# Optimization experiments

Measured on AMD Instinct MI355X. Metric: run time of the kernel, lower is better.

## Reference

```python
import jax, jax.numpy as jnp
import numpy as np

RMS_EPS = 1e-6


def setup_inputs() -> dict:
    key = jax.random.key(0)
    ks = jax.random.split(key, 6)
    B, S, D, F, E = 4, 2048, 1024, 4096, 8
    scale = 0.02
    return {
        "hidden_states": jax.random.normal(ks[0], (B, S, D), dtype=jnp.float32),
        "norm_weight": jnp.ones((D,), dtype=jnp.float32),
        "gate_w": jax.random.normal(ks[1], (E, D), dtype=jnp.float32) * scale,
        "w1": jax.random.normal(ks[2], (E, D, F), dtype=jnp.float32) * scale,
        "w3": jax.random.normal(ks[3], (E, D, F), dtype=jnp.float32) * scale,
        "w2": jax.random.normal(ks[4], (E, F, D), dtype=jnp.float32) * scale,
        "top_k": 2,
    }


def reference(hidden_states, norm_weight, gate_w, w1, w3, w2, top_k):
    B, S, D = hidden_states.shape
    E = gate_w.shape[0]
    # norm_fn: RMSNorm (pre-MoE norm in Mixtral block)
    x = hidden_states * jax.lax.rsqrt(jnp.mean(jnp.square(hidden_states), axis=-1, keepdims=True) + RMS_EPS)
    x = (x * norm_weight).reshape(-1, D)  # [T, D], T = B*S
    # router
    router_logits = jnp.einsum('td,ed->te', x, gate_w)  # [T, E]
    routing = jax.nn.softmax(router_logits.astype(jnp.float32), axis=-1)
    top_w, top_idx = jax.lax.top_k(routing, top_k)  # [T, k]
    top_w = top_w / jnp.sum(top_w, axis=-1, keepdims=True)
    top_w = top_w.astype(x.dtype)
    # dense-masked expert combine: tokens not routed to expert e get weight 0,
    # mathematically identical to the gather/scatter loop in the original.
    out = jnp.zeros_like(x)
    for e in range(E):  # fixed small loop over experts
        w_e = jnp.sum(jnp.where(top_idx == e, top_w, 0.0), axis=-1)  # [T]
        h = jax.nn.silu(x @ w1[e]) * (x @ w3[e])  # [T, F] SwiGLU expert
        out = out + w_e[:, None] * (h @ w2[e])
    return out.reshape(B, S, D), router_logits
```

## Files before the change

### kernel.cpp

```cpp
#include <hip/hip_runtime.h>
#include <hip/hip_bf16.h>

#define T_TOK 8192
#define D_DIM 1024
#define F_DIM 4096
#define E_NUM 8

typedef short s16x8 __attribute__((ext_vector_type(8)));
typedef float f32x4 __attribute__((ext_vector_type(4)));
typedef unsigned short u16x8 __attribute__((ext_vector_type(8)));

__device__ __forceinline__ unsigned short f2bf(float f) {
  union { float f; unsigned int u; } v; v.f = f;
  unsigned int u = v.u;
  return (unsigned short)((u + 0x7FFFu + ((u >> 16) & 1u)) >> 16);
}

__device__ __forceinline__ void async16(const void* g, void* l) {
  __builtin_amdgcn_global_load_lds((const __attribute__((address_space(1))) void*)g,
                                   (__attribute__((address_space(3))) void*)l, 16, 0, 0);
}

__global__ __launch_bounds__(256) void prepass_kernel(
    const float* __restrict__ hs, const float* __restrict__ nw,
    const float* __restrict__ gw, const float* __restrict__ w1,
    const float* __restrict__ w3, const float* __restrict__ w2,
    unsigned short* __restrict__ xb, unsigned short* __restrict__ w13t,
    unsigned short* __restrict__ w2t, float* __restrict__ logits_out,
    int* __restrict__ cnt, int* __restrict__ ilist, float* __restrict__ wlist) {
  __shared__ unsigned short tileS[64][72];
  __shared__ float red[4];
  __shared__ float pl[4][8];
  int bx = blockIdx.x;
  int tid = threadIdx.x;
  if (bx < 24576) {
    int tensor = bx >> 13;
    int e = (bx >> 10) & 7;
    int tl = bx & 1023;
    const float* src; int C, tr, tc;
    if (tensor == 0) {
      src = w1 + (size_t)e * D_DIM * F_DIM; C = F_DIM; tr = tl >> 6; tc = tl & 63;
    } else if (tensor == 1) {
      src = w3 + (size_t)e * D_DIM * F_DIM; C = F_DIM; tr = tl >> 6; tc = tl & 63;
    } else {
      src = w2 + (size_t)e * F_DIM * D_DIM; C = D_DIM; tr = tl >> 4; tc = tl & 15;
    }
    int r0 = tr * 64, c0 = tc * 64;
    int rr = tid >> 4, ccb = (tid & 15) * 4;
#pragma unroll
    for (int i = 0; i < 4; ++i) {
      int r = rr + i * 16;
      float4 v = *(const float4*)(src + (size_t)(r0 + r) * C + c0 + ccb);
      tileS[ccb + 0][r] = f2bf(v.x);
      tileS[ccb + 1][r] = f2bf(v.y);
      tileS[ccb + 2][r] = f2bf(v.z);
      tileS[ccb + 3][r] = f2bf(v.w);
    }
    __syncthreads();
    int row = tid >> 2, col = (tid & 3) * 16;
    unsigned short* dp;
    if (tensor < 2) {
      int f = c0 + row;
      int prow = ((f >> 5) * 64) + (f & 31) + (tensor == 1 ? 32 : 0);
      dp = w13t + ((size_t)e * 8192 + prow) * D_DIM + r0 + col;
    } else {
      dp = w2t + ((size_t)e * D_DIM + c0 + row) * F_DIM + r0 + col;
    }
    u16x8 v0, v1;
#pragma unroll
    for (int j = 0; j < 8; ++j) { v0[j] = tileS[row][col + j]; v1[j] = tileS[row][col + 8 + j]; }
    *(u16x8*)dp = v0;
    *(u16x8*)(dp + 8) = v1;
  } else {
    int t = bx - 24576;
    int lane = tid & 63, wid = tid >> 6;
    float4 v = ((const float4*)(hs + (size_t)t * D_DIM))[tid];
    float ss = v.x * v.x + v.y * v.y + v.z * v.z + v.w * v.w;
#pragma unroll
    for (int o = 32; o > 0; o >>= 1) ss += __shfl_xor(ss, o);
    if (lane == 0) red[wid] = ss;
    __syncthreads();
    float ms = (red[0] + red[1] + red[2] + red[3]) * (1.0f / 1024.0f);
    float rs = rsqrtf(ms + 1e-6f);
    float4 wv = ((const float4*)nw)[tid];
    float x0 = v.x * rs * wv.x, x1 = v.y * rs * wv.y;
    float x2 = v.z * rs * wv.z, x3 = v.w * rs * wv.w;
    ((ushort4*)(xb + (size_t)t * D_DIM))[tid] =
        make_ushort4(f2bf(x0), f2bf(x1), f2bf(x2), f2bf(x3));
    float p[8];
#pragma unroll
    for (int e = 0; e < 8; ++e) {
      float4 g = ((const float4*)(gw + (size_t)e * D_DIM))[tid];
      p[e] = x0 * g.x + x1 * g.y + x2 * g.z + x3 * g.w;
    }
#pragma unroll
    for (int e = 0; e < 8; ++e) {
#pragma unroll
      for (int o = 32; o > 0; o >>= 1) p[e] += __shfl_xor(p[e], o);
    }
    if (lane == 0) {
#pragma unroll
      for (int e = 0; e < 8; ++e) pl[wid][e] = p[e];
    }
    __syncthreads();
    if (tid == 0) {
      float l[8];
#pragma unroll
      for (int e = 0; e < 8; ++e) {
        l[e] = pl[0][e] + pl[1][e] + pl[2][e] + pl[3][e];
        logits_out[(size_t)t * 8 + e] = l[e];
      }
      int i0 = 0; float b0 = l[0];
#pragma unroll
      for (int e = 1; e < 8; ++e) if (l[e] > b0) { b0 = l[e]; i0 = e; }
      int i1 = (i0 == 0) ? 1 : 0; float b1 = l[i1];
#pragma unroll
      for (int e = 0; e < 8; ++e) if (e != i0 && l[e] > b1) { b1 = l[e]; i1 = e; }
      float wa = 1.0f / (1.0f + __expf(b1 - b0));
      float wb = 1.0f / (1.0f + __expf(b0 - b1));
      int p0 = atomicAdd(&cnt[i0], 1);
      ilist[i0 * T_TOK + p0] = t * 2;     wlist[i0 * T_TOK + p0] = wa;
      int p1 = atomicAdd(&cnt[i1], 1);
      ilist[i1 * T_TOK + p1] = t * 2 + 1; wlist[i1 * T_TOK + p1] = wb;
    }
  }
}

__global__ __launch_bounds__(512, 2) void gemm1_kernel(
    const unsigned short* __restrict__ xb, const unsigned short* __restrict__ w13t,
    unsigned short* __restrict__ H, const int* __restrict__ cnt,
    const int* __restrict__ ilist) {
  int flat = blockIdx.x;
  int e = flat & 7;
  int widx = flat >> 3;
  int ne = cnt[e];
  int art = (ne + 255) >> 8;
  if (widx >= (art << 5)) return;
  int rt = widx % art;
  int ft = widx / art;
  int r0 = rt * 256;
  __shared__ __align__(16) unsigned short As[3 * 8192];
  __shared__ __align__(16) unsigned short Bs[3 * 8192];
  __shared__ int toks[256];
  int tid = threadIdx.x, lane = tid & 63, w = tid >> 6;
  if (tid < 256) toks[tid] = ilist[e * T_TOK + min(r0 + tid, ne - 1)];
  __syncthreads();
  const unsigned short* bpanel = w13t + ((size_t)e * 8192 + ft * 256) * D_DIM;
  int sr0 = tid >> 2, sr1 = sr0 + 128;
  int ch0 = (((tid & 3) ^ ((sr0 >> 1) & 3)) * 8);
  int ch1 = (((tid & 3) ^ ((sr1 >> 1) & 3)) * 8);
  const unsigned short* ap0 = xb + (size_t)(toks[sr0] >> 1) * D_DIM + ch0;
  const unsigned short* ap1 = xb + (size_t)(toks[sr1] >> 1) * D_DIM + ch1;
  const unsigned short* bp0 = bpanel + (size_t)sr0 * D_DIM + ch0;
  const unsigned short* bp1 = bpanel + (size_t)sr1 * D_DIM + ch1;
  int d0 = (sr0 * 32) + (tid & 3) * 8;
  int d1 = d0 + 4096;
  int wr = w >> 2, wc = w & 3;
  int lr = lane & 15, lc = lane >> 4;
  int aoff[8], boff[4];
#pragma unroll
  for (int m = 0; m < 8; ++m) {
    int row = wr * 128 + m * 16 + lr;
    aoff[m] = row * 32 + ((lc ^ ((row >> 1) & 3)) * 8);
  }
#pragma unroll
  for (int n = 0; n < 4; ++n) {
    int row = wc * 64 + n * 16 + lr;
    boff[n] = row * 32 + ((lc ^ ((row >> 1) & 3)) * 8);
  }
  f32x4 acc[8][4] = {};
  async16(ap0, &As[d0]); async16(ap1, &As[d1]);
  async16(bp0, &Bs[d0]); async16(bp1, &Bs[d1]);
  async16(ap0 + 32, &As[8192 + d0]); async16(ap1 + 32, &As[8192 + d1]);
  async16(bp0 + 32, &Bs[8192 + d0]); async16(bp1 + 32, &Bs[8192 + d1]);

#define G1_STEP(T_, BUF_, VMC_, DOST_)                                          \
  {                                                                             \
    asm volatile("s_waitcnt vmcnt(" VMC_ ")" ::: "memory");                     \
    __builtin_amdgcn_s_barrier();                                               \
    const unsigned short* Ab = &As[(BUF_) * 8192];                              \
    const unsigned short* Bb = &Bs[(BUF_) * 8192];                              \
    s16x8 a[8], b[4];                                                           \
    if (DOST_) {                                   \
      int nk = ((T_) + 2) * 32;                                                 \
      async16(ap0 + nk, &As[(((BUF_) + 2) % 3) * 8192 + d0]);                   \
      async16(ap1 + nk, &As[(((BUF_) + 2) % 3) * 8192 + d1]);                   \
    }                                                                           \
    _Pragma("unroll") for (int m = 0; m < 4; ++m)                               \
        a[m] = *(const s16x8*)(Ab + aoff[m]);                                   \
    _Pragma("unroll") for (int n = 0; n < 4; ++n)                               \
        b[n] = *(const s16x8*)(Bb + boff[n]);                                   \
    __builtin_amdgcn_s_setprio(1);                                              \
    _Pragma("unroll") for (int m = 0; m < 4; ++m)                               \
        _Pragma("unroll") for (int n = 0; n < 4; ++n)                           \
            acc[m][n] = __builtin_amdgcn_mfma_f32_16x16x32_bf16(                \
                a[m], b[n], acc[m][n], 0, 0, 0);                                \
    __builtin_amdgcn_s_setprio(0);                                              \
    if (DOST_) {                                   \
      int nk = ((T_) + 2) * 32;                                                 \
      async16(bp0 + nk, &Bs[(((BUF_) + 2) % 3) * 8192 + d0]);                   \
      async16(bp1 + nk, &Bs[(((BUF_) + 2) % 3) * 8192 + d1]);                   \
    }                                                                           \
    _Pragma("unroll") for (int m = 4; m < 8; ++m)                               \
        a[m] = *(const s16x8*)(Ab + aoff[m]);                                   \
    __builtin_amdgcn_s_setprio(1);                                              \
    _Pragma("unroll") for (int m = 4; m < 8; ++m)                               \
        _Pragma("unroll") for (int n = 0; n < 4; ++n)                           \
            acc[m][n] = __builtin_amdgcn_mfma_f32_16x16x32_bf16(                \
                a[m], b[n], acc[m][n], 0, 0, 0);                                \
    __builtin_amdgcn_s_setprio(0);                                              \
  }

  for (int tb = 0; tb < 30; tb += 3) {
    G1_STEP(tb, 0, "4", 1)
    G1_STEP(tb + 1, 1, "4", 1)
    G1_STEP(tb + 2, 2, "4", 1)
  }
  G1_STEP(30, 0, "4", 0)
  G1_STEP(31, 1, "0", 0)
#undef G1_STEP

  int g4 = lane >> 4, cl = lane & 15;
  int fbase = (4 * ft + wc) * 32;
#pragma unroll
  for (int m = 0; m < 8; ++m) {
#pragma unroll
    for (int j = 0; j < 4; ++j) {
      int rloc = wr * 128 + m * 16 + g4 * 4 + j;
      if (r0 + rloc < ne) {
        unsigned short* hp = H + (size_t)toks[rloc] * F_DIM + fbase + cl;
#pragma unroll
        for (int n = 0; n < 2; ++n) {
          float c1 = acc[m][n][j], c3 = acc[m][n + 2][j];
          float h = c1 / (1.0f + __expf(-c1)) * c3;
          hp[n * 16] = f2bf(h);
        }
      }
    }
  }
}

__global__ __launch_bounds__(512, 2) void gemm2_kernel(
    const unsigned short* __restrict__ H, const unsigned short* __restrict__ w2t,
    const int* __restrict__ cnt, const int* __restrict__ ilist,
    const float* __restrict__ wlist, float* __restrict__ out) {
  int flat = blockIdx.x;
  int e = flat & 7;
  int widx = flat >> 3;
  int ne = cnt[e];
  int art = (ne + 255) >> 8;
  if (widx >= (art << 2)) return;
  int rt = widx % art;
  int nt = widx / art;
  int r0 = rt * 256;
  __shared__ __align__(16) unsigned short As[3 * 8192];
  __shared__ __align__(16) unsigned short Bs[3 * 8192];
  __shared__ int toks[256];
  __shared__ float wts[256];
  int tid = threadIdx.x, lane = tid & 63, w = tid >> 6;
  if (tid < 256) {
    int idx = e * T_TOK + min(r0 + tid, ne - 1);
    toks[tid] = ilist[idx];
    wts[tid] = wlist[idx];
  }
  __syncthreads();
  const unsigned short* bpanel = w2t + ((size_t)e * D_DIM + nt * 256) * F_DIM;
  int sr0 = tid >> 2, sr1 = sr0 + 128;
  int ch0 = (((tid & 3) ^ ((sr0 >> 1) & 3)) * 8);
  int ch1 = (((tid & 3) ^ ((sr1 >> 1) & 3)) * 8);
  const unsigned short* ap0 = H + (size_t)toks[sr0] * F_DIM + ch0;
  const unsigned short* ap1 = H + (size_t)toks[sr1] * F_DIM + ch1;
  const unsigned short* bp0 = bpanel + (size_t)sr0 * F_DIM + ch0;
  const unsigned short* bp1 = bpanel + (size_t)sr1 * F_DIM + ch1;
  int d0 = (sr0 * 32) + (tid & 3) * 8;
  int d1 = d0 + 4096;
  int wr = w >> 2, wc = w & 3;
  int lr = lane & 15, lc = lane >> 4;
  int aoff[8], boff[4];
#pragma unroll
  for (int m = 0; m < 8; ++m) {
    int row = wr * 128 + m * 16 + lr;
    aoff[m] = row * 32 + ((lc ^ ((row >> 1) & 3)) * 8);
  }
#pragma unroll
  for (int n = 0; n < 4; ++n) {
    int row = wc * 64 + n * 16 + lr;
    boff[n] = row * 32 + ((lc ^ ((row >> 1) & 3)) * 8);
  }
  f32x4 acc[8][4] = {};
  async16(ap0, &As[d0]); async16(ap1, &As[d1]);
  async16(bp0, &Bs[d0]); async16(bp1, &Bs[d1]);
  async16(ap0 + 32, &As[8192 + d0]); async16(ap1 + 32, &As[8192 + d1]);
  async16(bp0 + 32, &Bs[8192 + d0]); async16(bp1 + 32, &Bs[8192 + d1]);

#define G2_STEP(T_, BUF_, VMC_, DOST_)                                          \
  {                                                                             \
    asm volatile("s_waitcnt vmcnt(" VMC_ ")" ::: "memory");                     \
    __builtin_amdgcn_s_barrier();                                               \
    const unsigned short* Ab = &As[(BUF_) * 8192];                              \
    const unsigned short* Bb = &Bs[(BUF_) * 8192];                              \
    s16x8 a[8], b[4];                                                           \
    if (DOST_) {                                                                \
      int nk = ((T_) + 2) * 32;                                                 \
      async16(ap0 + nk, &As[(((BUF_) + 2) % 3) * 8192 + d0]);                   \
      async16(ap1 + nk, &As[(((BUF_) + 2) % 3) * 8192 + d1]);                   \
    }                                                                           \
    _Pragma("unroll") for (int m = 0; m < 4; ++m)                               \
        a[m] = *(const s16x8*)(Ab + aoff[m]);                                   \
    _Pragma("unroll") for (int n = 0; n < 4; ++n)                               \
        b[n] = *(const s16x8*)(Bb + boff[n]);                                   \
    __builtin_amdgcn_s_setprio(1);                                              \
    _Pragma("unroll") for (int m = 0; m < 4; ++m)                               \
        _Pragma("unroll") for (int n = 0; n < 4; ++n)                           \
            acc[m][n] = __builtin_amdgcn_mfma_f32_16x16x32_bf16(                \
                a[m], b[n], acc[m][n], 0, 0, 0);                                \
    __builtin_amdgcn_s_setprio(0);                                              \
    if (DOST_) {                                                                \
      int nk = ((T_) + 2) * 32;                                                 \
      async16(bp0 + nk, &Bs[(((BUF_) + 2) % 3) * 8192 + d0]);                   \
      async16(bp1 + nk, &Bs[(((BUF_) + 2) % 3) * 8192 + d1]);                   \
    }                                                                           \
    _Pragma("unroll") for (int m = 4; m < 8; ++m)                               \
        a[m] = *(const s16x8*)(Ab + aoff[m]);                                   \
    __builtin_amdgcn_s_setprio(1);                                              \
    _Pragma("unroll") for (int m = 4; m < 8; ++m)                               \
        _Pragma("unroll") for (int n = 0; n < 4; ++n)                           \
            acc[m][n] = __builtin_amdgcn_mfma_f32_16x16x32_bf16(                \
                a[m], b[n], acc[m][n], 0, 0, 0);                                \
    __builtin_amdgcn_s_setprio(0);                                              \
  }

  for (int tb = 0; tb < 126; tb += 3) {
    G2_STEP(tb, 0, "4", 1)
    G2_STEP(tb + 1, 1, "4", 1)
    G2_STEP(tb + 2, 2, "4", 1)
  }
  G2_STEP(126, 0, "4", 0)
  G2_STEP(127, 1, "0", 0)
#undef G2_STEP

  int g4 = lane >> 4, cl = lane & 15;
#pragma unroll
  for (int m = 0; m < 8; ++m) {
#pragma unroll
    for (int j = 0; j < 4; ++j) {
      int rloc = wr * 128 + m * 16 + g4 * 4 + j;
      if (r0 + rloc < ne) {
        int tok = toks[rloc] >> 1;
        float ww = wts[rloc];
        float* op = out + (size_t)tok * D_DIM + nt * 256 + wc * 64 + cl;
#pragma unroll
        for (int n = 0; n < 4; ++n)
          unsafeAtomicAdd(op + n * 16, ww * acc[m][n][j]);
      }
    }
  }
}

extern "C" void kernel_launch(void* const* d_in, const int* in_sizes, int n_in,
                              void* d_out, int out_size, void* d_ws, size_t ws_size,
                              hipStream_t stream) {
  const float* hs = (const float*)d_in[0];
  const float* nw = (const float*)d_in[1];
  const float* gw = (const float*)d_in[2];
  const float* w1 = (const float*)d_in[3];
  const float* w3 = (const float*)d_in[4];
  const float* w2 = (const float*)d_in[5];
  float* out = (float*)d_out;
  float* logits_out = out + (size_t)T_TOK * D_DIM;

  char* ws = (char*)d_ws;
  unsigned short* xb   = (unsigned short*)(ws);
  unsigned short* w13t = (unsigned short*)(ws + 16777216ull);
  unsigned short* w2t  = (unsigned short*)(ws + 150994944ull);
  unsigned short* H    = (unsigned short*)(ws + 218103808ull);
  int*   ilist = (int*)(ws + 352321536ull);
  float* wlist = (float*)(ws + 352583680ull);
  int*   cnt   = (int*)(ws + 352845824ull);

  hipMemsetAsync(out, 0, (size_t)T_TOK * D_DIM * sizeof(float), stream);
  hipMemsetAsync(cnt, 0, E_NUM * sizeof(int), stream);
  prepass_kernel<<<24576 + T_TOK, 256, 0, stream>>>(
      hs, nw, gw, w1, w3, w2, xb, w13t, w2t, logits_out, cnt, ilist, wlist);
  gemm1_kernel<<<E_NUM * 32 * 32, 512, 0, stream>>>(xb, w13t, H, cnt, ilist);
  gemm2_kernel<<<E_NUM * 32 * 4, 512, 0, stream>>>(H, w2t, cnt, ilist, wlist, out);
}
```

Baseline: 821.0 us.

## Pre-swizzle expert weights into MFMA fragment order and load B directly to registers

The prepass now writes w13 and w2 in a fragment-major layout, so each lane's 16-byte MFMA B operand sits contiguously per 16-row group and k-step. Both GEMM kernels drop the shared-memory B tiles and issue direct global_load_dwordx4 into registers, keeping only the activation tile in LDS with a triple-buffered async pipeline. This removes the LDS traffic and bank pressure for weights and frees LDS, but exposes global load latency on the MFMA critical path with only a single-step lookahead. Each wave also now loads its own B fragments, with no sharing across waves that use the same columns.

```diff
diff --git a/kernel.cpp b/kernel.cpp
--- a/kernel.cpp
+++ b/kernel.cpp
@@ -62,15 +62,20 @@
     if (tensor < 2) {
       int f = c0 + row;
       int prow = ((f >> 5) * 64) + (f & 31) + (tensor == 1 ? 32 : 0);
-      dp = w13t + ((size_t)e * 8192 + prow) * D_DIM + r0 + col;
+      int d0 = r0 + col;
+      dp = w13t + (size_t)e * 8388608 + (size_t)(prow >> 4) * 16384 +
+           (d0 >> 5) * 512 + ((d0 >> 3) & 3) * 128 + (prow & 15) * 8;
     } else {
-      dp = w2t + ((size_t)e * D_DIM + c0 + row) * F_DIM + r0 + col;
+      int rowD = c0 + row;
+      int k0f = r0 + col;
+      dp = w2t + (size_t)e * 4194304 + (size_t)(rowD >> 4) * 65536 +
+           (k0f >> 5) * 512 + ((k0f >> 3) & 3) * 128 + (rowD & 15) * 8;
     }
     u16x8 v0, v1;
 #pragma unroll
     for (int j = 0; j < 8; ++j) { v0[j] = tileS[row][col + j]; v1[j] = tileS[row][col + 8 + j]; }
     *(u16x8*)dp = v0;
-    *(u16x8*)(dp + 8) = v1;
+    *(u16x8*)(dp + 128) = v1;
   } else {
     int t = bx - 24576;
     int lane = tid & 63, wid = tid >> 6;
@@ -125,6 +130,39 @@
     }
   }
 }
+
+#define BLOAD(B_, P_) \
+  asm volatile("global_load_dwordx4 %0, %1, off" : "=v"(B_) : "v"(P_));
+
+#define GX_STEP(T_, BUF_, VMC_, DOA_)                                           \
+  {                                                                             \
+    const unsigned short* pb0 = bfp0 + (T_) * 512;                              \
+    const unsigned short* pb1 = bfp1 + (T_) * 512;                              \
+    const unsigned short* pb2 = bfp2 + (T_) * 512;                              \
+    const unsigned short* pb3 = bfp3 + (T_) * 512;                              \
+    s16x8 b0, b1, b2, b3;                                                       \
+    BLOAD(b0, pb0) BLOAD(b1, pb1) BLOAD(b2, pb2) BLOAD(b3, pb3)                 \
+    if (DOA_) {                                                                 \
+      int nk = ((T_) + 2) * 32;                                                 \
+      async16(ap0 + nk, &As[(((BUF_) + 2) % 3) * 8192 + d0]);                   \
+      async16(ap1 + nk, &As[(((BUF_) + 2) % 3) * 8192 + d1]);                   \
+    }                                                                           \
+    const unsigned short* Ab = &As[(BUF_) * 8192];                              \
+    s16x8 a[8];                                                                 \
+    _Pragma("unroll") for (int m = 0; m < 8; ++m)                               \
+        a[m] = *(const s16x8*)(Ab + aoff[m]);                                   \
+    asm volatile("s_waitcnt vmcnt(" VMC_ ")" ::: "memory");                     \
+    __builtin_amdgcn_sched_barrier(0);                                          \
+    __builtin_amdgcn_s_setprio(1);                                              \
+    _Pragma("unroll") for (int m = 0; m < 8; ++m) {                             \
+      acc[m][0] = __builtin_amdgcn_mfma_f32_16x16x32_bf16(a[m], b0, acc[m][0], 0, 0, 0); \
+      acc[m][1] = __builtin_amdgcn_mfma_f32_16x16x32_bf16(a[m], b1, acc[m][1], 0, 0, 0); \
+      acc[m][2] = __builtin_amdgcn_mfma_f32_16x16x32_bf16(a[m], b2, acc[m][2], 0, 0, 0); \
+      acc[m][3] = __builtin_amdgcn_mfma_f32_16x16x32_bf16(a[m], b3, acc[m][3], 0, 0, 0); \
+    }                                                                           \
+    __builtin_amdgcn_s_setprio(0);                                              \
+    __builtin_amdgcn_s_barrier();                                               \
+  }
 
 __global__ __launch_bounds__(512, 2) void gemm1_kernel(
     const unsigned short* __restrict__ xb, const unsigned short* __restrict__ w13t,
@@ -140,85 +178,42 @@
   int ft = widx / art;
   int r0 = rt * 256;
   __shared__ __align__(16) unsigned short As[3 * 8192];
-  __shared__ __align__(16) unsigned short Bs[3 * 8192];
   __shared__ int toks[256];
   int tid = threadIdx.x, lane = tid & 63, w = tid >> 6;
   if (tid < 256) toks[tid] = ilist[e * T_TOK + min(r0 + tid, ne - 1)];
   __syncthreads();
-  const unsigned short* bpanel = w13t + ((size_t)e * 8192 + ft * 256) * D_DIM;
   int sr0 = tid >> 2, sr1 = sr0 + 128;
   int ch0 = (((tid & 3) ^ ((sr0 >> 1) & 3)) * 8);
   int ch1 = (((tid & 3) ^ ((sr1 >> 1) & 3)) * 8);
   const unsigned short* ap0 = xb + (size_t)(toks[sr0] >> 1) * D_DIM + ch0;
   const unsigned short* ap1 = xb + (size_t)(toks[sr1] >> 1) * D_DIM + ch1;
-  const unsigned short* bp0 = bpanel + (size_t)sr0 * D_DIM + ch0;
-  const unsigned short* bp1 = bpanel + (size_t)sr1 * D_DIM + ch1;
   int d0 = (sr0 * 32) + (tid & 3) * 8;
   int d1 = d0 + 4096;
   int wr = w >> 2, wc = w & 3;
   int lr = lane & 15, lc = lane >> 4;
-  int aoff[8], boff[4];
+  int aoff[8];
 #pragma unroll
   for (int m = 0; m < 8; ++m) {
     int row = wr * 128 + m * 16 + lr;
     aoff[m] = row * 32 + ((lc ^ ((row >> 1) & 3)) * 8);
   }
-#pragma unroll
-  for (int n = 0; n < 4; ++n) {
-    int row = wc * 64 + n * 16 + lr;
-    boff[n] = row * 32 + ((lc ^ ((row >> 1) & 3)) * 8);
-  }
+  const unsigned short* bbase = w13t + (size_t)e * 8388608 + (size_t)lane * 8;
+  const unsigned short* bfp0 = bbase + (size_t)(ft * 16 + wc * 4 + 0) * 16384;
+  const unsigned short* bfp1 = bbase + (size_t)(ft * 16 + wc * 4 + 1) * 16384;
+  const unsigned short* bfp2 = bbase + (size_t)(ft * 16 + wc * 4 + 2) * 16384;
+  const unsigned short* bfp3 = bbase + (size_t)(ft * 16 + wc * 4 + 3) * 16384;
   f32x4 acc[8][4] = {};
-  async16(ap0, &As[d0]); async16(ap1, &As[d1]);
-  async16(bp0, &Bs[d0]); async16(bp1, &Bs[d1]);
+  async16(ap0, &As[d0]);             async16(ap1, &As[d1]);
   async16(ap0 + 32, &As[8192 + d0]); async16(ap1 + 32, &As[8192 + d1]);
-  async16(bp0 + 32, &Bs[8192 + d0]); async16(bp1 + 32, &Bs[8192 + d1]);
-
-#define G1_STEP(T_, BUF_, VMC_, DOST_)                                          \
-  {                                                                             \
-    asm volatile("s_waitcnt vmcnt(" VMC_ ")" ::: "memory");                     \
-    __builtin_amdgcn_s_barrier();                                               \
-    const unsigned short* Ab = &As[(BUF_) * 8192];                              \
-    const unsigned short* Bb = &Bs[(BUF_) * 8192];                              \
-    s16x8 a[8], b[4];                                                           \
-    if (DOST_) {                                   \
-      int nk = ((T_) + 2) * 32;                                                 \
-      async16(ap0 + nk, &As[(((BUF_) + 2) % 3) * 8192 + d0]);                   \
-      async16(ap1 + nk, &As[(((BUF_) + 2) % 3) * 8192 + d1]);                   \
-    }                                                                           \
-    _Pragma("unroll") for (int m = 0; m < 4; ++m)                               \
-        a[m] = *(const s16x8*)(Ab + aoff[m]);                                   \
-    _Pragma("unroll") for (int n = 0; n < 4; ++n)                               \
-        b[n] = *(const s16x8*)(Bb + boff[n]);                                   \
-    __builtin_amdgcn_s_setprio(1);                                              \
-    _Pragma("unroll") for (int m = 0; m < 4; ++m)                               \
-        _Pragma("unroll") for (int n = 0; n < 4; ++n)                           \
-            acc[m][n] = __builtin_amdgcn_mfma_f32_16x16x32_bf16(                \
-                a[m], b[n], acc[m][n], 0, 0, 0);                                \
-    __builtin_amdgcn_s_setprio(0);                                              \
-    if (DOST_) {                                   \
-      int nk = ((T_) + 2) * 32;                                                 \
-      async16(bp0 + nk, &Bs[(((BUF_) + 2) % 3) * 8192 + d0]);                   \
-      async16(bp1 + nk, &Bs[(((BUF_) + 2) % 3) * 8192 + d1]);                   \
-    }                                                                           \
-    _Pragma("unroll") for (int m = 4; m < 8; ++m)                               \
-        a[m] = *(const s16x8*)(Ab + aoff[m]);                                   \
-    __builtin_amdgcn_s_setprio(1);                                              \
-    _Pragma("unroll") for (int m = 4; m < 8; ++m)                               \
-        _Pragma("unroll") for (int n = 0; n < 4; ++n)                           \
-            acc[m][n] = __builtin_amdgcn_mfma_f32_16x16x32_bf16(                \
-                a[m], b[n], acc[m][n], 0, 0, 0);                                \
-    __builtin_amdgcn_s_setprio(0);                                              \
-  }
-
+  asm volatile("s_waitcnt vmcnt(2)" ::: "memory");
+  __builtin_amdgcn_s_barrier();
   for (int tb = 0; tb < 30; tb += 3) {
-    G1_STEP(tb, 0, "4", 1)
-    G1_STEP(tb + 1, 1, "4", 1)
-    G1_STEP(tb + 2, 2, "4", 1)
-  }
-  G1_STEP(30, 0, "4", 0)
-  G1_STEP(31, 1, "0", 0)
-#undef G1_STEP
+    GX_STEP(tb, 0, "2", 1)
+    GX_STEP(tb + 1, 1, "2", 1)
+    GX_STEP(tb + 2, 2, "2", 1)
+  }
+  GX_STEP(30, 0, "0", 0)
+  GX_STEP(31, 1, "0", 0)
 
   int g4 = lane >> 4, cl = lane & 15;
   int fbase = (4 * ft + wc) * 32;
@@ -254,7 +249,6 @@
   int nt = widx / art;
   int r0 = rt * 256;
   __shared__ __align__(16) unsigned short As[3 * 8192];
-  __shared__ __align__(16) unsigned short Bs[3 * 8192];
   __shared__ int toks[256];
   __shared__ float wts[256];
   int tid = threadIdx.x, lane = tid & 63, w = tid >> 6;
@@ -264,80 +258,38 @@
     wts[tid] = wlist[idx];
   }
   __syncthreads();
-  const unsigned short* bpanel = w2t + ((size_t)e * D_DIM + nt * 256) * F_DIM;
   int sr0 = tid >> 2, sr1 = sr0 + 128;
   int ch0 = (((tid & 3) ^ ((sr0 >> 1) & 3)) * 8);
   int ch1 = (((tid & 3) ^ ((sr1 >> 1) & 3)) * 8);
   const unsigned short* ap0 = H + (size_t)toks[sr0] * F_DIM + ch0;
   const unsigned short* ap1 = H + (size_t)toks[sr1] * F_DIM + ch1;
-  const unsigned short* bp0 = bpanel + (size_t)sr0 * F_DIM + ch0;
-  const unsigned short* bp1 = bpanel + (size_t)sr1 * F_DIM + ch1;
   int d0 = (sr0 * 32) + (tid & 3) * 8;
   int d1 = d0 + 4096;
   int wr = w >> 2, wc = w & 3;
   int lr = lane & 15, lc = lane >> 4;
-  int aoff[8], boff[4];
+  int aoff[8];
 #pragma unroll
   for (int m = 0; m < 8; ++m) {
     int row = wr * 128 + m * 16 + lr;
     aoff[m] = row * 32 + ((lc ^ ((row >> 1) & 3)) * 8);
   }
-#pragma unroll
-  for (int n = 0; n < 4; ++n) {
-    int row = wc * 64 + n * 16 + lr;
-    boff[n] = row * 32 + ((lc ^ ((row >> 1) & 3)) * 8);
-  }
+  const unsigned short* bbase = w2t + (size_t)e * 4194304 + (size_t)lane * 8;
+  const unsigned short* bfp0 = bbase + (size_t)(nt * 16 + wc * 4 + 0) * 65536;
+  const unsigned short* bfp1 = bbase + (size_t)(nt * 16 + wc * 4 + 1) * 65536;
+  const unsigned short* bfp2 = bbase + (size_t)(nt * 16 + wc * 4 + 2) * 65536;
+  const unsigned short* bfp3 = bbase + (size_t)(nt * 16 + wc * 4 + 3) * 65536;
   f32x4 acc[8][4] = {};
-  async16(ap0, &As[d0]); async16(ap1, &As[d1]);
-  async16(bp0, &Bs[d0]); async16(bp1, &Bs[d1]);
+  async16(ap0, &As[d0]);             async16(ap1, &As[d1]);
   async16(ap0 + 32, &As[8192 + d0]); async16(ap1 + 32, &As[8192 + d1]);
-  async16(bp0 + 32, &Bs[8192 + d0]); async16(bp1 + 32, &Bs[8192 + d1]);
-
-#define G2_STEP(T_, BUF_, VMC_, DOST_)                                          \
-  {                                                                             \
-    asm volatile("s_waitcnt vmcnt(" VMC_ ")" ::: "memory");                     \
-    __builtin_amdgcn_s_barrier();                                               \
-    const unsigned short* Ab = &As[(BUF_) * 8192];                              \
-    const unsigned short* Bb = &Bs[(BUF_) * 8192];                              \
-    s16x8 a[8], b[4];                                                           \
-    if (DOST_) {                                                                \
-      int nk = ((T_) + 2) * 32;                                                 \
-      async16(ap0 + nk, &As[(((BUF_) + 2) % 3) * 8192 + d0]);                   \
-      async16(ap1 + nk, &As[(((BUF_) + 2) % 3) * 8192 + d1]);                   \
-    }                                                                           \
-    _Pragma("unroll") for (int m = 0; m < 4; ++m)                               \
-        a[m] = *(const s16x8*)(Ab + aoff[m]);                                   \
-    _Pragma("unroll") for (int n = 0; n < 4; ++n)                               \
-        b[n] = *(const s16x8*)(Bb + boff[n]);                                   \
-    __builtin_amdgcn_s_setprio(1);                                              \
-    _Pragma("unroll") for (int m = 0; m < 4; ++m)                               \
-        _Pragma("unroll") for (int n = 0; n < 4; ++n)                           \
-            acc[m][n] = __builtin_amdgcn_mfma_f32_16x16x32_bf16(                \
-                a[m], b[n], acc[m][n], 0, 0, 0);                                \
-    __builtin_amdgcn_s_setprio(0);                                              \
-    if (DOST_) {                                                                \
-      int nk = ((T_) + 2) * 32;                                                 \
-      async16(bp0 + nk, &Bs[(((BUF_) + 2) % 3) * 8192 + d0]);                   \
-      async16(bp1 + nk, &Bs[(((BUF_) + 2) % 3) * 8192 + d1]);                   \
-    }                                                                           \
-    _Pragma("unroll") for (int m = 4; m < 8; ++m)                               \
-        a[m] = *(const s16x8*)(Ab + aoff[m]);                                   \
-    __builtin_amdgcn_s_setprio(1);                                              \
-    _Pragma("unroll") for (int m = 4; m < 8; ++m)                               \
-        _Pragma("unroll") for (int n = 0; n < 4; ++n)                           \
-            acc[m][n] = __builtin_amdgcn_mfma_f32_16x16x32_bf16(                \
-                a[m], b[n], acc[m][n], 0, 0, 0);                                \
-    __builtin_amdgcn_s_setprio(0);                                              \
-  }
-
+  asm volatile("s_waitcnt vmcnt(2)" ::: "memory");
+  __builtin_amdgcn_s_barrier();
   for (int tb = 0; tb < 126; tb += 3) {
-    G2_STEP(tb, 0, "4", 1)
-    G2_STEP(tb + 1, 1, "4", 1)
-    G2_STEP(tb + 2, 2, "4", 1)
-  }
-  G2_STEP(126, 0, "4", 0)
-  G2_STEP(127, 1, "0", 0)
-#undef G2_STEP
+    GX_STEP(tb, 0, "2", 1)
+    GX_STEP(tb + 1, 1, "2", 1)
+    GX_STEP(tb + 2, 2, "2", 1)
+  }
+  GX_STEP(126, 0, "0", 0)
+  GX_STEP(127, 1, "0", 0)
 
   int g4 = lane >> 4, cl = lane & 15;
 #pragma unroll
```

After: 997.1 us. 1.21x slower.
